# Performance work log

Measured on AMD Instinct MI355X. Metric: run time of the kernel, lower is better.

The kernel has to match this reference:

```python
import jax, jax.numpy as jnp
import numpy as np

LEAK = 0.1
K = 16  # nsample


def _gather(points, idx):
    # points: [B, N2, C], idx: [B, N1, K] -> [B, N1, K, C]
    return jax.vmap(lambda p, i: p[i])(points, idx)


def setup_inputs() -> dict:
    key = jax.random.key(0)
    ks = jax.random.split(key, 32)
    B, N1, N2, C = 2, 4096, 8192, 64
    M = [64, 64, 64]
    d = {}
    d['xyz1'] = jax.random.normal(ks[0], (B, 3, N1), dtype=jnp.float32)
    d['xyz2'] = jax.random.normal(ks[1], (B, 3, N2), dtype=jnp.float32)
    d['points1'] = jax.random.normal(ks[2], (B, C, N1), dtype=jnp.float32)
    d['points2'] = jax.random.normal(ks[3], (B, C, N2), dtype=jnp.float32)
    d['knn1'] = jax.random.normal(ks[4], (B, C, N1), dtype=jnp.float32)
    d['knn2'] = jax.random.normal(ks[5], (B, C, N2), dtype=jnp.float32)
    s = 0.05
    # fuse 1x1 Conv1d weights (no bias): [out=M0, in=C]
    for j, nm in enumerate(['Wfr', 'Wfro', 'Wfz', 'Wfr2', 'Wfro2', 'Wfz2']):
        d[nm] = jax.random.normal(ks[6 + j], (M[0], C), dtype=jnp.float32) * s
    # mlp 1x1 Conv2d weights/biases: layer0 in=3, then M[i-1]
    ins = [3, M[0], M[1]]
    k = 12
    for br in ['r', 'z', 'h']:
        for i in range(3):
            d['W%s%d' % (br, i)] = jax.random.normal(ks[k], (M[i], ins[i]), dtype=jnp.float32) * s
            d['b%s%d' % (br, i)] = jax.random.normal(ks[k + 1], (M[i],), dtype=jnp.float32) * s
            k += 2
    return d


def _forward(xyz1, xyz2, points1, points2, knn1, knn2,
             Wfr, Wfro, Wfz, Wfr2, Wfro2, Wfz2,
             Wr0, br0, Wr1, br1, Wr2, br2,
             Wz0, bz0, Wz1, bz1, Wz2, bz2,
             Wh0, bh0, Wh1, bh1, Wh2, bh2):
    leaky = lambda x: jax.nn.leaky_relu(x, LEAK)
    conv = lambda x, W, b: jnp.einsum('bnkc,oc->bnko', x, W) + b
    fuse = lambda p, W: jnp.einsum('oc,bcn->bno', W, p)  # [B,N,Cout]

    x1 = jnp.transpose(xyz1, (0, 2, 1))   # [B,N1,3]
    x2 = jnp.transpose(xyz2, (0, 2, 1))   # [B,N2,3]
    f1 = jnp.transpose(knn1, (0, 2, 1))   # [B,N1,Ck]
    f2 = jnp.transpose(knn2, (0, 2, 1))   # [B,N2,Ck]

    # cosine knn on feature space (smallest distance = largest similarity)
    f1n = f1 / jnp.sqrt(jnp.sum(f1 * f1, -1, keepdims=True) + 1e-8)
    f2n = f2 / jnp.sqrt(jnp.sum(f2 * f2, -1, keepdims=True) + 1e-8)
    cdist = 1.0 - jnp.einsum('bnc,bmc->bnm', f1n, f2n)
    _, idx_c = jax.lax.top_k(-cdist, K // 2)
    # euclidean knn on xyz
    sq = (jnp.sum(x1 * x1, -1)[:, :, None] + jnp.sum(x2 * x2, -1)[:, None, :]
          - 2.0 * jnp.einsum('bnc,bmc->bnm', x1, x2))
    _, idx_p = jax.lax.top_k(-sq, K // 2)
    idx = jnp.concatenate([idx_c, idx_p], axis=-1)  # [B,N1,K]

    p2r = fuse(points2, Wfr2)    # [B,N2,M0]
    p2ro = fuse(points2, Wfro2)
    p2z = fuse(points2, Wfz2)
    g_r = _gather(p2r, idx)      # [B,N1,K,M0]
    g_ro = _gather(p2ro, idx)
    g_z = _gather(p2z, idx)
    dirx = _gather(x2, idx) - x1[:, :, None, :]  # [B,N1,K,3]

    # r gate
    gp1r = fuse(points1, Wfr)[:, :, None, :]
    r = leaky(conv(dirx, Wr0, br0) + gp1r + g_r)
    r = leaky(conv(r, Wr1, br1))
    r = jax.nn.sigmoid(conv(r, Wr2, br2))          # [B,N1,K,M2]

    # z gate (max over K before last layer)
    gp1z = fuse(points1, Wfz)[:, :, None, :]
    z = leaky(conv(dirx, Wz0, bz0) + gp1z + g_ro)
    z = jnp.max(leaky(conv(z, Wz1, bz1)), axis=2, keepdims=True)
    z = jax.nn.sigmoid(conv(z, Wz2, bz2))[:, :, 0, :]  # [B,N1,M2]

    # h candidate; note: original code's `if self.relu:` is always truthy
    # (self.relu holds the LeakyReLU module), so final activation is LeakyReLU.
    p1o = fuse(points1, Wfro)                       # [B,N1,M0]
    p1e = r * p1o[:, :, None, :]
    h = leaky(conv(dirx, Wh0, bh0) + p1e + g_z)
    h = jnp.max(leaky(conv(h, Wh1, bh1)), axis=2, keepdims=True)
    h = leaky(conv(h, Wh2, bh2))[:, :, 0, :]        # [B,N1,M2]

    out = (1.0 - z) * p1o + z * h                   # [B,N1,M2]
    return jnp.transpose(out, (0, 2, 1))            # [B,M2,N1]


def reference(xyz1, xyz2, points1, points2, knn1, knn2,
              Wfr, Wfro, Wfz, Wfr2, Wfro2, Wfz2,
              Wr0, br0, Wr1, br1, Wr2, br2,
              Wz0, bz0, Wz1, bz1, Wz2, bz2,
              Wh0, bh0, Wh1, bh1, Wh2, bh2):
    return _forward(xyz1, xyz2, points1, points2, knn1, knn2,
                    Wfr, Wfro, Wfz, Wfr2, Wfro2, Wfz2,
                    Wr0, br0, Wr1, br1, Wr2, br2,
                    Wz0, bz0, Wz1, bz1, Wz2, bz2,
                    Wh0, bh0, Wh1, bh1, Wh2, bh2)
```

## Files before the change

kernel.cpp:

```cpp
#include <hip/hip_runtime.h>
#include <math.h>

#define NB 2
#define NN1 4096
#define NN2 8192
#define NPART 8
#define LEAKK 0.1f

typedef unsigned long long u64k;

__device__ __forceinline__ float leaky_(float x) { return fmaxf(x, LEAKK * x); }
__device__ __forceinline__ float sigm_(float x) { return 1.0f / (1.0f + __expf(-x)); }

__device__ __forceinline__ void insq_(u64k k, u64k* q) {
#pragma unroll
  for (int j = 7; j > 0; --j)
    q[j] = (k < q[j - 1]) ? q[j - 1] : ((k < q[j]) ? k : q[j]);
  q[0] = (k < q[0]) ? k : q[0];
}

__device__ __forceinline__ void merge8q_(u64k* a, u64k* b) {
  u64k r[8];
#pragma unroll
  for (int s = 0; s < 8; ++s) {
    bool ta = a[0] < b[0];
    r[s] = ta ? a[0] : b[0];
#pragma unroll
    for (int j = 0; j < 7; ++j) {
      a[j] = ta ? a[j + 1] : a[j];
      b[j] = ta ? b[j] : b[j + 1];
    }
  }
#pragma unroll
  for (int j = 0; j < 8; ++j) a[j] = r[j];
}

__global__ void prep_w_kernel(const float* s0, const float* s1, const float* s2,
                              const float* s3, const float* s4, const float* s5,
                              const float* s6, const float* s7, const float* s8,
                              const float* s9, const float* s10, const float* s11,
                              const float* s12, const float* s13, const float* s14,
                              float* wt) {
  const float* srcs[15] = {s0, s1, s2, s3, s4, s5, s6, s7, s8, s9, s10, s11, s12, s13, s14};
  int bid = blockIdx.x;
  const float* src = srcs[bid];
  int cols = (bid < 6) ? 64 : (((bid - 6) % 3 == 0) ? 3 : 64);
  float* dst = wt + bid * 4096;
  for (int e = threadIdx.x; e < 64 * cols; e += blockDim.x) {
    int o = e / cols, c = e - o * cols;
    dst[c * 64 + o] = src[e];
  }
}

__global__ __launch_bounds__(64) void prep_side_kernel(const float* knn, const float* xyz,
                                                       float* fdst, float* xdst, int N) {
  __shared__ float T[64 * 65];
  __shared__ float rs[64];
  int b = blockIdx.y;
  int n0 = blockIdx.x * 64;
  int l = threadIdx.x;
  const float* kb = knn + (size_t)b * 64 * N + n0;
  for (int c = 0; c < 64; ++c) T[c * 65 + l] = kb[(size_t)c * N + l];
  __syncthreads();
  float s = 0.f;
  for (int c = 0; c < 64; ++c) { float v = T[c * 65 + l]; s += v * v; }
  rs[l] = 1.0f / sqrtf(s + 1e-8f);
  __syncthreads();
  for (int i = 0; i < 64; ++i)
    fdst[(size_t)(b * N + n0 + i) * 64 + l] = T[l * 65 + i] * rs[i];
  const float* xb = xyz + (size_t)b * 3 * N + n0;
  float x = xb[l], y = xb[N + l], z = xb[2 * N + l];
  ((float4*)xdst)[b * N + n0 + l] = make_float4(x, y, z, x * x + y * y + z * z);
}

__global__ __launch_bounds__(256) void fuse_kernel(const float* pts, const float* wt0,
                                                   const float* wt1, const float* wt2,
                                                   float* d0, float* d1, float* d2, int N) {
  int b = blockIdx.y;
  int w = threadIdx.x >> 6, l = threadIdx.x & 63;
  int n = blockIdx.x * 4 + w;
  const float* pb = pts + (size_t)b * 64 * N + n;
  float a0 = 0.f, a1 = 0.f, a2 = 0.f;
  for (int c = 0; c < 64; ++c) {
    float p = pb[(size_t)c * N];
    a0 += p * wt0[c * 64 + l];
    a1 += p * wt1[c * 64 + l];
    a2 += p * wt2[c * 64 + l];
  }
  size_t ob = (size_t)(b * N + n) * 64 + l;
  d0[ob] = a0; d1[ob] = a1; d2[ob] = a2;
}

__global__ __launch_bounds__(256, 3) void knn_kernel(const float* f1n, const float* f2n,
                                                     const float* x1t, const float* x2t,
                                                     u64k* pq) {
  __shared__ __align__(16) float SH[13120];
  float* f1t = SH;
  float* f2d = SH + 4096;
  float* x1x = SH + 12352;
  float* x1y = SH + 12416;
  float* x1z = SH + 12480;
  float* x1w = SH + 12544;
  float* x2s = SH + 12608;

  int t = threadIdx.x;
  int lane = t & 63, w = t >> 6;
  int n0 = blockIdx.x * 64;
  int part = (int)blockIdx.y;
  int b = (int)blockIdx.z;

  {
    const float* f1row = f1n + (size_t)(b * NN1 + n0 + lane) * 64;
#pragma unroll
    for (int pass = 0; pass < 4; ++pass) {
      int c0 = pass * 16 + w * 4;
      float4 v = *(const float4*)(f1row + c0);
      f1t[(c0 + 0) * 64 + lane] = v.x;
      f1t[(c0 + 1) * 64 + lane] = v.y;
      f1t[(c0 + 2) * 64 + lane] = v.z;
      f1t[(c0 + 3) * 64 + lane] = v.w;
    }
    if (t < 64) {
      float4 v = ((const float4*)x1t)[b * NN1 + n0 + t];
      x1x[t] = v.x; x1y[t] = v.y; x1z[t] = v.z; x1w[t] = v.w;
    }
  }

  u64k cq[8], eq[8];
#pragma unroll
  for (int j = 0; j < 8; ++j) { cq[j] = ~0ull; eq[j] = ~0ull; }

  int ty = t >> 4, tx = t & 15;
  __syncthreads();
  float xx = x1x[lane], xy = x1y[lane], xz = x1z[lane], xw = x1w[lane];

  for (int ch = 0; ch < 8; ++ch) {
    int cc = part * 1024 + ch * 128;

    {
      int cand = t & 127;
      int sb = (t >> 7) * 8;
      const float* src = f2n + (size_t)(b * NN2 + cc + cand) * 64 + sb * 4;
#pragma unroll
      for (int p = 0; p < 8; ++p) {
        float4 v = *(const float4*)(src + p * 4);
        int c0 = (sb + p) * 4;
        f2d[(c0 + 0) * 128 + cand] = v.x;
        f2d[(c0 + 1) * 128 + cand] = v.y;
        f2d[(c0 + 2) * 128 + cand] = v.z;
        f2d[(c0 + 3) * 128 + cand] = v.w;
      }
      if (t < 128) ((float4*)x2s)[t] = ((const float4*)x2t)[b * NN2 + cc + t];
    }
    __syncthreads();

    float acc0[4][4], acc1[4][4];
#pragma unroll
    for (int i = 0; i < 4; ++i)
#pragma unroll
      for (int j = 0; j < 4; ++j) { acc0[i][j] = 0.f; acc1[i][j] = 0.f; }

#pragma unroll 2
    for (int k = 0; k < 64; ++k) {
      float4 a  = *(const float4*)&f1t[k * 64 + ty * 4];
      float4 b0 = *(const float4*)&f2d[k * 128 + tx * 4];
      float4 b1 = *(const float4*)&f2d[k * 128 + 64 + tx * 4];
      acc0[0][0] += a.x * b0.x; acc0[0][1] += a.x * b0.y; acc0[0][2] += a.x * b0.z; acc0[0][3] += a.x * b0.w;
      acc0[1][0] += a.y * b0.x; acc0[1][1] += a.y * b0.y; acc0[1][2] += a.y * b0.z; acc0[1][3] += a.y * b0.w;
      acc0[2][0] += a.z * b0.x; acc0[2][1] += a.z * b0.y; acc0[2][2] += a.z * b0.z; acc0[2][3] += a.z * b0.w;
      acc0[3][0] += a.w * b0.x; acc0[3][1] += a.w * b0.y; acc0[3][2] += a.w * b0.z; acc0[3][3] += a.w * b0.w;
      acc1[0][0] += a.x * b1.x; acc1[0][1] += a.x * b1.y; acc1[0][2] += a.x * b1.z; acc1[0][3] += a.x * b1.w;
      acc1[1][0] += a.y * b1.x; acc1[1][1] += a.y * b1.y; acc1[1][2] += a.y * b1.z; acc1[1][3] += a.y * b1.w;
      acc1[2][0] += a.z * b1.x; acc1[2][1] += a.z * b1.y; acc1[2][2] += a.z * b1.z; acc1[2][3] += a.z * b1.w;
      acc1[3][0] += a.w * b1.x; acc1[3][1] += a.w * b1.y; acc1[3][2] += a.w * b1.z; acc1[3][3] += a.w * b1.w;
    }
    __syncthreads();

#pragma unroll
    for (int i = 0; i < 4; ++i) {
      int r = ty * 4 + i;
#pragma unroll
      for (int j = 0; j < 4; ++j) {
        f2d[r * 129 + tx * 4 + j]      = fmaxf(1.f - acc0[i][j], 0.f);
        f2d[r * 129 + 64 + tx * 4 + j] = fmaxf(1.f - acc1[i][j], 0.f);
      }
    }
    __syncthreads();

    {
      const float* drow = &f2d[lane * 129 + w * 32];
      const float4* x2q = ((const float4*)x2s) + w * 32;
#pragma unroll 4
      for (int j = 0; j < 32; ++j) {
        unsigned gi = cc + w * 32 + j;
        float dv = drow[j];
        u64k kc = ((u64k)__float_as_uint(dv) << 32) | gi;
        if (kc < cq[7]) insq_(kc, cq);
        float4 xv = x2q[j];
        float d3 = fmaxf(xw + xv.w - 2.f * (xx * xv.x + xy * xv.y + xz * xv.z), 0.f);
        u64k ke = ((u64k)__float_as_uint(d3) << 32) | gi;
        if (ke < eq[7]) insq_(ke, eq);
      }
    }
    __syncthreads();
  }

  {
    u64k* Lc = (u64k*)SH;
    u64k* Le = ((u64k*)SH) + 2112;
#pragma unroll
    for (int j = 0; j < 8; ++j) {
      Lc[lane * 33 + w * 8 + j] = cq[j];
      Le[lane * 33 + w * 8 + j] = eq[j];
    }
    __syncthreads();
    if (t < 128) {
      int typ = t >> 6, r = t & 63;
      const u64k* L = typ ? Le : Lc;
      u64k a0[8], a1[8], a2[8], a3[8];
#pragma unroll
      for (int j = 0; j < 8; ++j) {
        a0[j] = L[r * 33 + 0 + j];
        a1[j] = L[r * 33 + 8 + j];
        a2[j] = L[r * 33 + 16 + j];
        a3[j] = L[r * 33 + 24 + j];
      }
      merge8q_(a0, a1);
      merge8q_(a2, a3);
      merge8q_(a0, a2);
      size_t base = ((size_t)((b * NPART + part) * NN1) + n0 + r) * 16 + typ * 8;
#pragma unroll
      for (int j = 0; j < 8; ++j) pq[base + j] = a0[j];
    }
  }
}

__device__ __forceinline__ void loadq_(const u64k* pq, int b, int p, int n1, int typ, u64k* q) {
  size_t base = ((size_t)((b * NPART + p) * NN1) + n1) * 16 + typ * 8;
#pragma unroll
  for (int j = 0; j < 8; ++j) q[j] = pq[base + j];
}

__global__ __launch_bounds__(256) void merge_parts_kernel(const u64k* pq, int* idxb) {
  int g = blockIdx.x * blockDim.x + threadIdx.x;
  if (g >= NB * NN1) return;
  int b = g / NN1, n1 = g - b * NN1;
#pragma unroll
  for (int typ = 0; typ < 2; ++typ) {
    u64k A[8], B[8], C[8], D[8];
    loadq_(pq, b, 0, n1, typ, A);
    loadq_(pq, b, 1, n1, typ, B);
    merge8q_(A, B);
    loadq_(pq, b, 2, n1, typ, C);
    loadq_(pq, b, 3, n1, typ, D);
    merge8q_(C, D);
    merge8q_(A, C);
    loadq_(pq, b, 4, n1, typ, B);
    loadq_(pq, b, 5, n1, typ, C);
    merge8q_(B, C);
    loadq_(pq, b, 6, n1, typ, C);
    loadq_(pq, b, 7, n1, typ, D);
    merge8q_(C, D);
    merge8q_(B, C);
    merge8q_(A, B);
    size_t ob = (size_t)g * 16 + typ * 8;
#pragma unroll
    for (int j = 0; j < 8; ++j) idxb[ob + j] = (int)(A[j] & 0xffffffffull);
  }
}

__device__ __forceinline__ void mat64_(const float* src, const float* Wt, float bias,
                                       int l, float* acc) {
#pragma unroll
  for (int k = 0; k < 16; ++k) acc[k] = bias;
#pragma unroll
  for (int cb = 0; cb < 4; ++cb) {
    float wv[16];
#pragma unroll
    for (int i = 0; i < 16; ++i) wv[i] = Wt[(cb * 16 + i) * 64 + l];
#pragma unroll
    for (int k = 0; k < 16; ++k) {
      float4 a0 = *(const float4*)&src[k * 64 + cb * 16 + 0];
      float4 a1 = *(const float4*)&src[k * 64 + cb * 16 + 4];
      float4 a2 = *(const float4*)&src[k * 64 + cb * 16 + 8];
      float4 a3 = *(const float4*)&src[k * 64 + cb * 16 + 12];
      acc[k] += wv[0] * a0.x + wv[1] * a0.y + wv[2] * a0.z + wv[3] * a0.w
              + wv[4] * a1.x + wv[5] * a1.y + wv[6] * a1.z + wv[7] * a1.w
              + wv[8] * a2.x + wv[9] * a2.y + wv[10] * a2.z + wv[11] * a2.w
              + wv[12] * a3.x + wv[13] * a3.y + wv[14] * a3.z + wv[15] * a3.w;
    }
  }
}

__device__ __forceinline__ float matv64_(const float* v, const float* Wt, float bias, int l) {
  float acc = bias;
#pragma unroll
  for (int cb = 0; cb < 4; ++cb) {
    float4 v0 = *(const float4*)&v[cb * 16 + 0];
    float4 v1 = *(const float4*)&v[cb * 16 + 4];
    float4 v2 = *(const float4*)&v[cb * 16 + 8];
    float4 v3 = *(const float4*)&v[cb * 16 + 12];
    acc += Wt[(cb * 16 + 0) * 64 + l] * v0.x + Wt[(cb * 16 + 1) * 64 + l] * v0.y
         + Wt[(cb * 16 + 2) * 64 + l] * v0.z + Wt[(cb * 16 + 3) * 64 + l] * v0.w
         + Wt[(cb * 16 + 4) * 64 + l] * v1.x + Wt[(cb * 16 + 5) * 64 + l] * v1.y
         + Wt[(cb * 16 + 6) * 64 + l] * v1.z + Wt[(cb * 16 + 7) * 64 + l] * v1.w
         + Wt[(cb * 16 + 8) * 64 + l] * v2.x + Wt[(cb * 16 + 9) * 64 + l] * v2.y
         + Wt[(cb * 16 + 10) * 64 + l] * v2.z + Wt[(cb * 16 + 11) * 64 + l] * v2.w
         + Wt[(cb * 16 + 12) * 64 + l] * v3.x + Wt[(cb * 16 + 13) * 64 + l] * v3.y
         + Wt[(cb * 16 + 14) * 64 + l] * v3.z + Wt[(cb * 16 + 15) * 64 + l] * v3.w;
  }
  return acc;
}

__global__ __launch_bounds__(256, 3) void gru_kernel(
    const int* idxb, const float* x1t, const float* x2t,
    const float* p1r, const float* p1ro, const float* p1z,
    const float* p2r, const float* p2ro, const float* p2z,
    const float* wt,
    const float* br0, const float* br1, const float* br2,
    const float* bz0, const float* bz1, const float* bz2,
    const float* bh0, const float* bh1, const float* bh2,
    float* out) {
  __shared__ float As[4][16 * 64];
  __shared__ float Bs[4][16 * 64];
  __shared__ float Rs[4][16 * 64];
  __shared__ float Vs[4][64];
  __shared__ float dxs[4][16 * 4];
  __shared__ int idxs[4][16];

  int t = threadIdx.x;
  int w = t >> 6, l = t & 63;
  int b = blockIdx.y;
  int n1i = blockIdx.x * 4 + w;
  int rowbase = b * NN1 + n1i;

  float* A = As[w]; float* Bf = Bs[w]; float* R3 = Rs[w];
  float* V = Vs[w]; float* dx = dxs[w];
  int* idxw = idxs[w];

  if (l < 16) {
    int gi = idxb[(size_t)rowbase * 16 + l];
    idxw[l] = gi;
    float4 x1v = ((const float4*)x1t)[rowbase];
    float4 x2v = ((const float4*)x2t)[b * NN2 + gi];
    dx[l * 4 + 0] = x2v.x - x1v.x;
    dx[l * 4 + 1] = x2v.y - x1v.y;
    dx[l * 4 + 2] = x2v.z - x1v.z;
    dx[l * 4 + 3] = 0.f;
  }
  float pr  = p1r[(size_t)rowbase * 64 + l];
  float pro = p1ro[(size_t)rowbase * 64 + l];
  float pz  = p1z[(size_t)rowbase * 64 + l];

  const float* Wr0t = wt + 6 * 4096;
  const float* Wr1t = wt + 7 * 4096;
  const float* Wr2t = wt + 8 * 4096;
  const float* Wz0t = wt + 9 * 4096;
  const float* Wz1t = wt + 10 * 4096;
  const float* Wz2t = wt + 11 * 4096;
  const float* Wh0t = wt + 12 * 4096;
  const float* Wh1t = wt + 13 * 4096;
  const float* Wh2t = wt + 14 * 4096;

  float acc[16];

  {
    float w0 = Wr0t[l], w1 = Wr0t[64 + l], w2 = Wr0t[128 + l], b0 = br0[l];
#pragma unroll
    for (int k = 0; k < 16; ++k) {
      int gk = idxw[k];
      float g = p2r[((size_t)b * NN2 + gk) * 64 + l];
      float4 dxk = *(const float4*)&dx[k * 4];
      A[k * 64 + l] = leaky_(b0 + pr + g + w0 * dxk.x + w1 * dxk.y + w2 * dxk.z);
    }
  }
  mat64_(A, Wr1t, br1[l], l, acc);
#pragma unroll
  for (int k = 0; k < 16; ++k) Bf[k * 64 + l] = leaky_(acc[k]);
  mat64_(Bf, Wr2t, br2[l], l, acc);
#pragma unroll
  for (int k = 0; k < 16; ++k) R3[k * 64 + l] = sigm_(acc[k]);

  {
    float w0 = Wz0t[l], w1 = Wz0t[64 + l], w2 = Wz0t[128 + l], b0 = bz0[l];
#pragma unroll
    for (int k = 0; k < 16; ++k) {
      int gk = idxw[k];
      float g = p2ro[((size_t)b * NN2 + gk) * 64 + l];
      float4 dxk = *(const float4*)&dx[k * 4];
      A[k * 64 + l] = leaky_(b0 + pz + g + w0 * dxk.x + w1 * dxk.y + w2 * dxk.z);
    }
  }
  mat64_(A, Wz1t, bz1[l], l, acc);
  {
    float zm = -INFINITY;
#pragma unroll
    for (int k = 0; k < 16; ++k) zm = fmaxf(zm, leaky_(acc[k]));
    V[l] = zm;
  }
  float z3 = sigm_(matv64_(V, Wz2t, bz2[l], l));

  {
    float w0 = Wh0t[l], w1 = Wh0t[64 + l], w2 = Wh0t[128 + l], b0 = bh0[l];
#pragma unroll
    for (int k = 0; k < 16; ++k) {
      int gk = idxw[k];
      float g = p2z[((size_t)b * NN2 + gk) * 64 + l];
      float4 dxk = *(const float4*)&dx[k * 4];
      A[k * 64 + l] = leaky_(b0 + R3[k * 64 + l] * pro + g + w0 * dxk.x + w1 * dxk.y + w2 * dxk.z);
    }
  }
  mat64_(A, Wh1t, bh1[l], l, acc);
  {
    float hm = -INFINITY;
#pragma unroll
    for (int k = 0; k < 16; ++k) hm = fmaxf(hm, leaky_(acc[k]));
    V[l] = hm;
  }
  float h3 = leaky_(matv64_(V, Wh2t, bh2[l], l));

  out[((size_t)b * 64 + l) * NN1 + n1i] = (1.0f - z3) * pro + z3 * h3;
}

extern "C" void kernel_launch(void* const* d_in, const int* in_sizes, int n_in,
                              void* d_out, int out_size, void* d_ws, size_t ws_size,
                              hipStream_t stream) {
  (void)in_sizes; (void)n_in; (void)out_size; (void)ws_size;
  const float* xyz1    = (const float*)d_in[0];
  const float* xyz2    = (const float*)d_in[1];
  const float* points1 = (const float*)d_in[2];
  const float* points2 = (const float*)d_in[3];
  const float* knn1    = (const float*)d_in[4];
  const float* knn2    = (const float*)d_in[5];
  const float* Wfr   = (const float*)d_in[6];
  const float* Wfro  = (const float*)d_in[7];
  const float* Wfz   = (const float*)d_in[8];
  const float* Wfr2  = (const float*)d_in[9];
  const float* Wfro2 = (const float*)d_in[10];
  const float* Wfz2  = (const float*)d_in[11];
  const float* Wr0 = (const float*)d_in[12]; const float* br0 = (const float*)d_in[13];
  const float* Wr1 = (const float*)d_in[14]; const float* br1 = (const float*)d_in[15];
  const float* Wr2 = (const float*)d_in[16]; const float* br2 = (const float*)d_in[17];
  const float* Wz0 = (const float*)d_in[18]; const float* bz0 = (const float*)d_in[19];
  const float* Wz1 = (const float*)d_in[20]; const float* bz1 = (const float*)d_in[21];
  const float* Wz2 = (const float*)d_in[22]; const float* bz2 = (const float*)d_in[23];
  const float* Wh0 = (const float*)d_in[24]; const float* bh0 = (const float*)d_in[25];
  const float* Wh1 = (const float*)d_in[26]; const float* bh1 = (const float*)d_in[27];
  const float* Wh2 = (const float*)d_in[28]; const float* bh2 = (const float*)d_in[29];

  float* W = (float*)d_ws;
  size_t o = 0;
  float* f1n = W + o; o += (size_t)NB * NN1 * 64;
  float* f2n = W + o; o += (size_t)NB * NN2 * 64;
  float* x1t = W + o; o += (size_t)NB * NN1 * 4;
  float* x2t = W + o; o += (size_t)NB * NN2 * 4;
  float* p1r = W + o; o += (size_t)NB * NN1 * 64;
  float* p1ro = W + o; o += (size_t)NB * NN1 * 64;
  float* p1z = W + o; o += (size_t)NB * NN1 * 64;
  float* p2r = W + o; o += (size_t)NB * NN2 * 64;
  float* p2ro = W + o; o += (size_t)NB * NN2 * 64;
  float* p2z = W + o; o += (size_t)NB * NN2 * 64;
  float* wt = W + o; o += (size_t)15 * 4096;
  u64k* pq = (u64k*)(W + o); o += (size_t)2 * NB * NPART * NN1 * 16;
  int* idxb = (int*)(W + o); o += (size_t)NB * NN1 * 16;

  float* out = (float*)d_out;

  hipLaunchKernelGGL(prep_w_kernel, dim3(15), dim3(256), 0, stream,
                     Wfr, Wfro, Wfz, Wfr2, Wfro2, Wfz2,
                     Wr0, Wr1, Wr2, Wz0, Wz1, Wz2, Wh0, Wh1, Wh2, wt);
  hipLaunchKernelGGL(prep_side_kernel, dim3(NN1 / 64, NB), dim3(64), 0, stream,
                     knn1, xyz1, f1n, x1t, NN1);
  hipLaunchKernelGGL(prep_side_kernel, dim3(NN2 / 64, NB), dim3(64), 0, stream,
                     knn2, xyz2, f2n, x2t, NN2);
  hipLaunchKernelGGL(fuse_kernel, dim3(NN1 / 4, NB), dim3(256), 0, stream,
                     points1, wt + 0 * 4096, wt + 1 * 4096, wt + 2 * 4096,
                     p1r, p1ro, p1z, NN1);
  hipLaunchKernelGGL(fuse_kernel, dim3(NN2 / 4, NB), dim3(256), 0, stream,
                     points2, wt + 3 * 4096, wt + 4 * 4096, wt + 5 * 4096,
                     p2r, p2ro, p2z, NN2);
  hipLaunchKernelGGL(knn_kernel, dim3(NN1 / 64, NPART, NB), dim3(256), 0, stream,
                     f1n, f2n, x1t, x2t, pq);
  hipLaunchKernelGGL(merge_parts_kernel, dim3((NB * NN1 + 255) / 256), dim3(256), 0, stream,
                     pq, idxb);
  hipLaunchKernelGGL(gru_kernel, dim3(NN1 / 4, NB), dim3(256), 0, stream,
                     idxb, x1t, x2t, p1r, p1ro, p1z, p2r, p2ro, p2z, wt,
                     br0, br1, br2, bz0, bz1, bz2, bh0, bh1, bh2, out);
}
```

Baseline: 607.8 us.

## Retile GRU MLPs as block GEMMs, split KNN into more parts, widen prep

```diff
diff --git a/kernel.cpp b/kernel.cpp
--- a/kernel.cpp
+++ b/kernel.cpp
@@ -4,8 +4,11 @@
 #define NB 2
 #define NN1 4096
 #define NN2 8192
-#define NPART 8
+#define NPART 16
+#define PARTSZ (NN2 / NPART)
+#define NCHUNK (PARTSZ / 128)
 #define LEAKK 0.1f
+#define GPAD 68
 
 typedef unsigned long long u64k;
 
@@ -52,25 +55,37 @@
   }
 }
 
-__global__ __launch_bounds__(64) void prep_side_kernel(const float* knn, const float* xyz,
-                                                       float* fdst, float* xdst, int N) {
+__global__ __launch_bounds__(256) void prep_side_kernel(const float* knn, const float* xyz,
+                                                        float* fdst, float* xdst, int N) {
   __shared__ float T[64 * 65];
-  __shared__ float rs[64];
+  __shared__ float ps[4 * 64];
   int b = blockIdx.y;
   int n0 = blockIdx.x * 64;
-  int l = threadIdx.x;
+  int t = threadIdx.x, w = t >> 6, l = t & 63;
   const float* kb = knn + (size_t)b * 64 * N + n0;
-  for (int c = 0; c < 64; ++c) T[c * 65 + l] = kb[(size_t)c * N + l];
+#pragma unroll
+  for (int i = 0; i < 16; ++i) {
+    int c = w * 16 + i;
+    T[c * 65 + l] = kb[(size_t)c * N + l];
+  }
   __syncthreads();
   float s = 0.f;
-  for (int c = 0; c < 64; ++c) { float v = T[c * 65 + l]; s += v * v; }
-  rs[l] = 1.0f / sqrtf(s + 1e-8f);
-  __syncthreads();
-  for (int i = 0; i < 64; ++i)
-    fdst[(size_t)(b * N + n0 + i) * 64 + l] = T[l * 65 + i] * rs[i];
-  const float* xb = xyz + (size_t)b * 3 * N + n0;
-  float x = xb[l], y = xb[N + l], z = xb[2 * N + l];
-  ((float4*)xdst)[b * N + n0 + l] = make_float4(x, y, z, x * x + y * y + z * z);
+#pragma unroll
+  for (int i = 0; i < 16; ++i) { float v = T[(w * 16 + i) * 65 + l]; s += v * v; }
+  ps[w * 64 + l] = s;
+  __syncthreads();
+#pragma unroll
+  for (int i = 0; i < 16; ++i) {
+    int p = w * 16 + i;
+    float rsum = ps[p] + ps[64 + p] + ps[128 + p] + ps[192 + p];
+    float rs = 1.0f / sqrtf(rsum + 1e-8f);
+    fdst[(size_t)(b * N + n0 + p) * 64 + l] = T[l * 65 + p] * rs;
+  }
+  if (t < 64) {
+    const float* xb = xyz + (size_t)b * 3 * N + n0;
+    float x = xb[t], y = xb[N + t], z = xb[2 * N + t];
+    ((float4*)xdst)[b * N + n0 + t] = make_float4(x, y, z, x * x + y * y + z * z);
+  }
 }
 
 __global__ __launch_bounds__(256) void fuse_kernel(const float* pts, const float* wt0,
@@ -134,8 +149,8 @@
   __syncthreads();
   float xx = x1x[lane], xy = x1y[lane], xz = x1z[lane], xw = x1w[lane];
 
-  for (int ch = 0; ch < 8; ++ch) {
-    int cc = part * 1024 + ch * 128;
+  for (int ch = 0; ch < NCHUNK; ++ch) {
+    int cc = part * PARTSZ + ch * 128;
 
     {
       int cand = t & 127;
@@ -245,74 +260,37 @@
   int g = blockIdx.x * blockDim.x + threadIdx.x;
   if (g >= NB * NN1) return;
   int b = g / NN1, n1 = g - b * NN1;
-#pragma unroll
   for (int typ = 0; typ < 2; ++typ) {
-    u64k A[8], B[8], C[8], D[8];
+    u64k A[8], B[8];
     loadq_(pq, b, 0, n1, typ, A);
-    loadq_(pq, b, 1, n1, typ, B);
-    merge8q_(A, B);
-    loadq_(pq, b, 2, n1, typ, C);
-    loadq_(pq, b, 3, n1, typ, D);
-    merge8q_(C, D);
-    merge8q_(A, C);
-    loadq_(pq, b, 4, n1, typ, B);
-    loadq_(pq, b, 5, n1, typ, C);
-    merge8q_(B, C);
-    loadq_(pq, b, 6, n1, typ, C);
-    loadq_(pq, b, 7, n1, typ, D);
-    merge8q_(C, D);
-    merge8q_(B, C);
-    merge8q_(A, B);
+    for (int p = 1; p < NPART; ++p) {
+      loadq_(pq, b, p, n1, typ, B);
+      merge8q_(A, B);
+    }
     size_t ob = (size_t)g * 16 + typ * 8;
 #pragma unroll
     for (int j = 0; j < 8; ++j) idxb[ob + j] = (int)(A[j] & 0xffffffffull);
   }
 }
 
-__device__ __forceinline__ void mat64_(const float* src, const float* Wt, float bias,
-                                       int l, float* acc) {
-#pragma unroll
-  for (int k = 0; k < 16; ++k) acc[k] = bias;
-#pragma unroll
-  for (int cb = 0; cb < 4; ++cb) {
-    float wv[16];
-#pragma unroll
-    for (int i = 0; i < 16; ++i) wv[i] = Wt[(cb * 16 + i) * 64 + l];
-#pragma unroll
-    for (int k = 0; k < 16; ++k) {
-      float4 a0 = *(const float4*)&src[k * 64 + cb * 16 + 0];
-      float4 a1 = *(const float4*)&src[k * 64 + cb * 16 + 4];
-      float4 a2 = *(const float4*)&src[k * 64 + cb * 16 + 8];
-      float4 a3 = *(const float4*)&src[k * 64 + cb * 16 + 12];
-      acc[k] += wv[0] * a0.x + wv[1] * a0.y + wv[2] * a0.z + wv[3] * a0.w
-              + wv[4] * a1.x + wv[5] * a1.y + wv[6] * a1.z + wv[7] * a1.w
-              + wv[8] * a2.x + wv[9] * a2.y + wv[10] * a2.z + wv[11] * a2.w
-              + wv[12] * a3.x + wv[13] * a3.y + wv[14] * a3.z + wv[15] * a3.w;
-    }
-  }
-}
-
-__device__ __forceinline__ float matv64_(const float* v, const float* Wt, float bias, int l) {
-  float acc = bias;
-#pragma unroll
-  for (int cb = 0; cb < 4; ++cb) {
-    float4 v0 = *(const float4*)&v[cb * 16 + 0];
-    float4 v1 = *(const float4*)&v[cb * 16 + 4];
-    float4 v2 = *(const float4*)&v[cb * 16 + 8];
-    float4 v3 = *(const float4*)&v[cb * 16 + 12];
-    acc += Wt[(cb * 16 + 0) * 64 + l] * v0.x + Wt[(cb * 16 + 1) * 64 + l] * v0.y
-         + Wt[(cb * 16 + 2) * 64 + l] * v0.z + Wt[(cb * 16 + 3) * 64 + l] * v0.w
-         + Wt[(cb * 16 + 4) * 64 + l] * v1.x + Wt[(cb * 16 + 5) * 64 + l] * v1.y
-         + Wt[(cb * 16 + 6) * 64 + l] * v1.z + Wt[(cb * 16 + 7) * 64 + l] * v1.w
-         + Wt[(cb * 16 + 8) * 64 + l] * v2.x + Wt[(cb * 16 + 9) * 64 + l] * v2.y
-         + Wt[(cb * 16 + 10) * 64 + l] * v2.z + Wt[(cb * 16 + 11) * 64 + l] * v2.w
-         + Wt[(cb * 16 + 12) * 64 + l] * v3.x + Wt[(cb * 16 + 13) * 64 + l] * v3.y
-         + Wt[(cb * 16 + 14) * 64 + l] * v3.z + Wt[(cb * 16 + 15) * 64 + l] * v3.w;
-  }
-  return acc;
-}
-
-__global__ __launch_bounds__(256, 3) void gru_kernel(
+__device__ __forceinline__ void gemm64_(const float* Ain, const float* Wt,
+                                        int ty, int tx, float acc[4][4]) {
+#pragma unroll
+  for (int i = 0; i < 4; ++i)
+#pragma unroll
+    for (int j = 0; j < 4; ++j) acc[i][j] = 0.f;
+#pragma unroll 8
+  for (int c = 0; c < 64; ++c) {
+    float4 a  = *(const float4*)&Ain[c * GPAD + ty * 4];
+    float4 wv = *(const float4*)&Wt[c * 64 + tx * 4];
+    acc[0][0] += a.x * wv.x; acc[0][1] += a.x * wv.y; acc[0][2] += a.x * wv.z; acc[0][3] += a.x * wv.w;
+    acc[1][0] += a.y * wv.x; acc[1][1] += a.y * wv.y; acc[1][2] += a.y * wv.z; acc[1][3] += a.y * wv.w;
+    acc[2][0] += a.z * wv.x; acc[2][1] += a.z * wv.y; acc[2][2] += a.z * wv.z; acc[2][3] += a.z * wv.w;
+    acc[3][0] += a.w * wv.x; acc[3][1] += a.w * wv.y; acc[3][2] += a.w * wv.z; acc[3][3] += a.w * wv.w;
+  }
+}
+
+__global__ __launch_bounds__(256, 4) void gru_kernel(
     const int* idxb, const float* x1t, const float* x2t,
     const float* p1r, const float* p1ro, const float* p1z,
     const float* p2r, const float* p2ro, const float* p2z,
@@ -321,36 +299,32 @@
     const float* bz0, const float* bz1, const float* bz2,
     const float* bh0, const float* bh1, const float* bh2,
     float* out) {
-  __shared__ float As[4][16 * 64];
-  __shared__ float Bs[4][16 * 64];
-  __shared__ float Rs[4][16 * 64];
-  __shared__ float Vs[4][64];
-  __shared__ float dxs[4][16 * 4];
-  __shared__ int idxs[4][16];
+  __shared__ __align__(16) float A1[64 * GPAD];
+  __shared__ __align__(16) float A2[64 * GPAD];
+  __shared__ float Vpart[16 * 64];
+  __shared__ float dxs[64 * 4];
+  __shared__ int idxs[64];
 
   int t = threadIdx.x;
   int w = t >> 6, l = t & 63;
+  int ty = t >> 4, tx = t & 15;
   int b = blockIdx.y;
   int n1i = blockIdx.x * 4 + w;
   int rowbase = b * NN1 + n1i;
 
-  float* A = As[w]; float* Bf = Bs[w]; float* R3 = Rs[w];
-  float* V = Vs[w]; float* dx = dxs[w];
-  int* idxw = idxs[w];
-
   if (l < 16) {
     int gi = idxb[(size_t)rowbase * 16 + l];
-    idxw[l] = gi;
+    idxs[w * 16 + l] = gi;
     float4 x1v = ((const float4*)x1t)[rowbase];
     float4 x2v = ((const float4*)x2t)[b * NN2 + gi];
-    dx[l * 4 + 0] = x2v.x - x1v.x;
-    dx[l * 4 + 1] = x2v.y - x1v.y;
-    dx[l * 4 + 2] = x2v.z - x1v.z;
-    dx[l * 4 + 3] = 0.f;
-  }
-  float pr  = p1r[(size_t)rowbase * 64 + l];
+    dxs[(w * 16 + l) * 4 + 0] = x2v.x - x1v.x;
+    dxs[(w * 16 + l) * 4 + 1] = x2v.y - x1v.y;
+    dxs[(w * 16 + l) * 4 + 2] = x2v.z - x1v.z;
+    dxs[(w * 16 + l) * 4 + 3] = 0.f;
+  }
+  float pr  = p1r [(size_t)rowbase * 64 + l];
   float pro = p1ro[(size_t)rowbase * 64 + l];
-  float pz  = p1z[(size_t)rowbase * 64 + l];
+  float pz  = p1z [(size_t)rowbase * 64 + l];
 
   const float* Wr0t = wt + 6 * 4096;
   const float* Wr1t = wt + 7 * 4096;
@@ -362,62 +336,141 @@
   const float* Wh1t = wt + 13 * 4096;
   const float* Wh2t = wt + 14 * 4096;
 
-  float acc[16];
+  __syncthreads();
 
   {
     float w0 = Wr0t[l], w1 = Wr0t[64 + l], w2 = Wr0t[128 + l], b0 = br0[l];
 #pragma unroll
     for (int k = 0; k < 16; ++k) {
-      int gk = idxw[k];
-      float g = p2r[((size_t)b * NN2 + gk) * 64 + l];
-      float4 dxk = *(const float4*)&dx[k * 4];
-      A[k * 64 + l] = leaky_(b0 + pr + g + w0 * dxk.x + w1 * dxk.y + w2 * dxk.z);
-    }
-  }
-  mat64_(A, Wr1t, br1[l], l, acc);
-#pragma unroll
-  for (int k = 0; k < 16; ++k) Bf[k * 64 + l] = leaky_(acc[k]);
-  mat64_(Bf, Wr2t, br2[l], l, acc);
-#pragma unroll
-  for (int k = 0; k < 16; ++k) R3[k * 64 + l] = sigm_(acc[k]);
+      int row = w * 16 + k;
+      int gi = idxs[row];
+      float g = p2r[((size_t)b * NN2 + gi) * 64 + l];
+      float4 d = *(const float4*)&dxs[row * 4];
+      A1[l * GPAD + row] = leaky_(b0 + pr + g + w0 * d.x + w1 * d.y + w2 * d.z);
+    }
+  }
+  __syncthreads();
+
+  float acc[4][4];
+
+  gemm64_(A1, Wr1t, ty, tx, acc);
+  {
+    const float* bq = &br1[tx * 4];
+#pragma unroll
+    for (int j = 0; j < 4; ++j) {
+      float bb = bq[j];
+#pragma unroll
+      for (int i = 0; i < 4; ++i)
+        A2[(tx * 4 + j) * GPAD + ty * 4 + i] = leaky_(acc[i][j] + bb);
+    }
+  }
+  __syncthreads();
+
+  gemm64_(A2, Wr2t, ty, tx, acc);
+  {
+    const float* bq = &br2[tx * 4];
+#pragma unroll
+    for (int j = 0; j < 4; ++j) {
+      float bb = bq[j];
+#pragma unroll
+      for (int i = 0; i < 4; ++i)
+        A1[(tx * 4 + j) * GPAD + ty * 4 + i] = sigm_(acc[i][j] + bb);
+    }
+  }
+  __syncthreads();
 
   {
     float w0 = Wz0t[l], w1 = Wz0t[64 + l], w2 = Wz0t[128 + l], b0 = bz0[l];
 #pragma unroll
     for (int k = 0; k < 16; ++k) {
-      int gk = idxw[k];
-      float g = p2ro[((size_t)b * NN2 + gk) * 64 + l];
-      float4 dxk = *(const float4*)&dx[k * 4];
-      A[k * 64 + l] = leaky_(b0 + pz + g + w0 * dxk.x + w1 * dxk.y + w2 * dxk.z);
-    }
-  }
-  mat64_(A, Wz1t, bz1[l], l, acc);
-  {
-    float zm = -INFINITY;
-#pragma unroll
-    for (int k = 0; k < 16; ++k) zm = fmaxf(zm, leaky_(acc[k]));
-    V[l] = zm;
-  }
-  float z3 = sigm_(matv64_(V, Wz2t, bz2[l], l));
+      int row = w * 16 + k;
+      int gi = idxs[row];
+      float g = p2ro[((size_t)b * NN2 + gi) * 64 + l];
+      float4 d = *(const float4*)&dxs[row * 4];
+      A2[l * GPAD + row] = leaky_(b0 + pz + g + w0 * d.x + w1 * d.y + w2 * d.z);
+    }
+  }
+  __syncthreads();
+
+  gemm64_(A2, Wz1t, ty, tx, acc);
+  {
+    const float* bq = &bz1[tx * 4];
+#pragma unroll
+    for (int j = 0; j < 4; ++j) {
+      float bb = bq[j];
+      float m = leaky_(acc[0][j] + bb);
+      m = fmaxf(m, leaky_(acc[1][j] + bb));
+      m = fmaxf(m, leaky_(acc[2][j] + bb));
+      m = fmaxf(m, leaky_(acc[3][j] + bb));
+      Vpart[ty * 64 + tx * 4 + j] = m;
+    }
+  }
+  __syncthreads();
+  float vm;
+  {
+    float v0 = Vpart[(w * 4 + 0) * 64 + l];
+    float v1 = Vpart[(w * 4 + 1) * 64 + l];
+    float v2 = Vpart[(w * 4 + 2) * 64 + l];
+    float v3 = Vpart[(w * 4 + 3) * 64 + l];
+    vm = fmaxf(fmaxf(v0, v1), fmaxf(v2, v3));
+  }
+  __syncthreads();
+  float* Vv = Vpart;
+  Vv[w * 64 + l] = vm;
+  __syncthreads();
+  float z3;
+  {
+    float a = bz2[l];
+#pragma unroll 8
+    for (int c = 0; c < 64; ++c) a += Vv[w * 64 + c] * Wz2t[c * 64 + l];
+    z3 = sigm_(a);
+  }
 
   {
     float w0 = Wh0t[l], w1 = Wh0t[64 + l], w2 = Wh0t[128 + l], b0 = bh0[l];
 #pragma unroll
     for (int k = 0; k < 16; ++k) {
-      int gk = idxw[k];
-      float g = p2z[((size_t)b * NN2 + gk) * 64 + l];
-      float4 dxk = *(const float4*)&dx[k * 4];
-      A[k * 64 + l] = leaky_(b0 + R3[k * 64 + l] * pro + g + w0 * dxk.x + w1 * dxk.y + w2 * dxk.z);
-    }
-  }
-  mat64_(A, Wh1t, bh1[l], l, acc);
-  {
-    float hm = -INFINITY;
-#pragma unroll
-    for (int k = 0; k < 16; ++k) hm = fmaxf(hm, leaky_(acc[k]));
-    V[l] = hm;
-  }
-  float h3 = leaky_(matv64_(V, Wh2t, bh2[l], l));
+      int row = w * 16 + k;
+      int gi = idxs[row];
+      float g = p2z[((size_t)b * NN2 + gi) * 64 + l];
+      float4 d = *(const float4*)&dxs[row * 4];
+      float r3 = A1[l * GPAD + row];
+      A2[l * GPAD + row] = leaky_(b0 + r3 * pro + g + w0 * d.x + w1 * d.y + w2 * d.z);
+    }
+  }
+  __syncthreads();
+
+  gemm64_(A2, Wh1t, ty, tx, acc);
+  {
+    const float* bq = &bh1[tx * 4];
+#pragma unroll
+    for (int j = 0; j < 4; ++j) {
+      float bb = bq[j];
+      float m = leaky_(acc[0][j] + bb);
+      m = fmaxf(m, leaky_(acc[1][j] + bb));
+      m = fmaxf(m, leaky_(acc[2][j] + bb));
+      m = fmaxf(m, leaky_(acc[3][j] + bb));
+      Vpart[ty * 64 + tx * 4 + j] = m;
+    }
+  }
+  __syncthreads();
+  {
+    float v0 = Vpart[(w * 4 + 0) * 64 + l];
+    float v1 = Vpart[(w * 4 + 1) * 64 + l];
+    float v2 = Vpart[(w * 4 + 2) * 64 + l];
+    float v3 = Vpart[(w * 4 + 3) * 64 + l];
+    vm = fmaxf(fmaxf(v0, v1), fmaxf(v2, v3));
+  }
+  __syncthreads();
+  Vv[w * 64 + l] = vm;
+  __syncthreads();
+  float h3;
+  {
+    float a = bh2[l];
+#pragma unroll 8
+    for (int c = 0; c < 64; ++c) a += Vv[w * 64 + c] * Wh2t[c * 64 + l];
+    h3 = leaky_(a);
+  }
 
   out[((size_t)b * 64 + l) * NN1 + n1i] = (1.0f - z3) * pro + z3 * h3;
 }
@@ -469,9 +522,9 @@
   hipLaunchKernelGGL(prep_w_kernel, dim3(15), dim3(256), 0, stream,
                      Wfr, Wfro, Wfz, Wfr2, Wfro2, Wfz2,
                      Wr0, Wr1, Wr2, Wz0, Wz1, Wz2, Wh0, Wh1, Wh2, wt);
-  hipLaunchKernelGGL(prep_side_kernel, dim3(NN1 / 64, NB), dim3(64), 0, stream,
+  hipLaunchKernelGGL(prep_side_kernel, dim3(NN1 / 64, NB), dim3(256), 0, stream,
                      knn1, xyz1, f1n, x1t, NN1);
-  hipLaunchKernelGGL(prep_side_kernel, dim3(NN2 / 64, NB), dim3(64), 0, stream,
+  hipLaunchKernelGGL(prep_side_kernel, dim3(NN2 / 64, NB), dim3(256), 0, stream,
                      knn2, xyz2, f2n, x2t, NN2);
   hipLaunchKernelGGL(fuse_kernel, dim3(NN1 / 4, NB), dim3(256), 0, stream,
                      points1, wt + 0 * 4096, wt + 1 * 4096, wt + 2 * 4096,
```

Result: faster. 578.9 us (-4.8%).
